# Kernel optimization log

Hardware: AMD Instinct MI355X
Metric: run time of the kernel (lower is better)

## Reference

```python
import jax, jax.numpy as jnp
import numpy as np

CH = 128
GROUPS = 8
HEADS = 8
HEAD_DIM = CH // HEADS  # 16
EPS = 1e-5


def setup_inputs() -> dict:
    key = jax.random.key(0)
    ks = jax.random.split(key, 5)
    x = jax.random.normal(ks[0], (8, CH, 128, 128), dtype=jnp.float32)
    gn_w = jnp.ones((CH,), dtype=jnp.float32)
    gn_b = jnp.zeros((CH,), dtype=jnp.float32)
    w_in = jax.random.normal(ks[1], (CH, CH), dtype=jnp.float32) * (1.0 / np.sqrt(CH))
    b_in = jax.random.normal(ks[2], (CH,), dtype=jnp.float32) * 0.01
    w_out = jax.random.normal(ks[3], (CH, CH), dtype=jnp.float32) * (1.0 / np.sqrt(CH))
    b_out = jax.random.normal(ks[4], (CH,), dtype=jnp.float32) * 0.01
    return {"x": x, "gn_w": gn_w, "gn_b": gn_b, "w_in": w_in, "b_in": b_in,
            "w_out": w_out, "b_out": b_out}


def _group_norm(x, gamma, beta):
    b, c, H, W = x.shape
    xg = x.reshape(b, GROUPS, c // GROUPS, H, W)
    mean = xg.mean(axis=(2, 3, 4), keepdims=True)
    var = xg.var(axis=(2, 3, 4), keepdims=True)
    xg = (xg - mean) * jax.lax.rsqrt(var + EPS)
    x = xg.reshape(b, c, H, W)
    return x * gamma[None, :, None, None] + beta[None, :, None, None]


def _conv1x1(x, w, bias):
    # w: [out_c, in_c] (1x1 conv == pointwise matmul over channels)
    return jnp.einsum('oc,bchw->bohw', w, x) + bias[None, :, None, None]


def reference(x, gn_w, gn_b, w_in, b_in, w_out, b_out):
    b, c, H, W = x.shape
    h = _group_norm(x, gn_w, gn_b)
    h = _conv1x1(h, w_in, b_in)
    # reshape to [b, heads, head_dim, H*W]; attention over head_dim axis,
    # contracting the spatial axis (d = H*W) as in the original einsums
    hh = h.reshape(b, HEADS, HEAD_DIM, H * W)
    scale = HEAD_DIM ** (-0.5)
    scores = jnp.einsum('bhid,bhjd->bhij', hh, hh) * scale  # [b,heads,hd,hd]
    weights = jax.nn.softmax(scores, axis=-1)
    attn = jnp.einsum('bhij,bhjd->bhid', weights, hh)
    attn = attn.reshape(b, c, H, W)
    h = _conv1x1(attn, w_out, b_out)
    return x + h
```

## Files before the change

kernel.cpp:

```cpp
#include <hip/hip_runtime.h>


#define NPOS 16384

typedef short short8 __attribute__((ext_vector_type(8)));
typedef float f32x4 __attribute__((ext_vector_type(4)));

__device__ __forceinline__ unsigned short f2bf(float f) {
    union { float f; unsigned u; } v; v.f = f;
    unsigned r = (v.u + 0x7fffu + ((v.u >> 16) & 1u)) >> 16;
    return (unsigned short)r;
}
__device__ __forceinline__ float bf2f(unsigned short u) {
    union { unsigned u; float f; } v; v.u = ((unsigned)u) << 16;
    return v.f;
}

__global__ __launch_bounds__(256, 2) void k_gram(const float* __restrict__ x,
                                                 float* __restrict__ G,
                                                 float* __restrict__ mv) {
    __shared__ unsigned short Xs[128 * 256];

    const int t = threadIdx.x;
    const int lane = t & 63, wv = t >> 6;
    const int q = lane >> 4, i16 = lane & 15;
    const int b = blockIdx.x >> 6;
    const int d0 = (blockIdx.x & 63) << 8;

    const float* xb = x + (size_t)b * (128 * NPOS) + d0;
#pragma unroll
    for (int i = 0; i < 32; ++i) {
        int idx = t + i * 256;
        int c = idx >> 6, d4 = idx & 63;
        float4 v = *((const float4*)(xb + (size_t)c * NPOS) + d4);
        ushort4 o;
        o.x = f2bf(v.x); o.y = f2bf(v.y); o.z = f2bf(v.z); o.w = f2bf(v.w);
        int g = d4 >> 1;
        int sg = g ^ (c & 7);
        *(ushort4*)&Xs[c * 256 + (sg << 3) + ((d4 & 1) << 2)] = o;
    }
    __syncthreads();

    f32x4 acc[2][8];
    f32x4 macc[2];
#pragma unroll
    for (int a = 0; a < 2; ++a) {
        macc[a] = (f32x4){0.f, 0.f, 0.f, 0.f};
#pragma unroll
        for (int ct = 0; ct < 8; ++ct) acc[a][ct] = (f32x4){0.f, 0.f, 0.f, 0.f};
    }
    const short8 ones = {(short)0x3F80, (short)0x3F80, (short)0x3F80, (short)0x3F80,
                         (short)0x3F80, (short)0x3F80, (short)0x3F80, (short)0x3F80};
    const int r0 = wv * 32 + i16, r1 = r0 + 16;
#pragma unroll
    for (int ks = 0; ks < 8; ++ks) {
        int g = ks * 4 + q;
        short8 a0 = *(const short8*)&Xs[r0 * 256 + ((g ^ (r0 & 7)) << 3)];
        short8 a1 = *(const short8*)&Xs[r1 * 256 + ((g ^ (r1 & 7)) << 3)];
        macc[0] = __builtin_amdgcn_mfma_f32_16x16x32_bf16(a0, ones, macc[0], 0, 0, 0);
        macc[1] = __builtin_amdgcn_mfma_f32_16x16x32_bf16(a1, ones, macc[1], 0, 0, 0);
#pragma unroll
        for (int ct = 0; ct < 8; ++ct) {
            int rb = ct * 16 + i16;
            short8 bb = *(const short8*)&Xs[rb * 256 + ((g ^ (rb & 7)) << 3)];
            acc[0][ct] = __builtin_amdgcn_mfma_f32_16x16x32_bf16(a0, bb, acc[0][ct], 0, 0, 0);
            acc[1][ct] = __builtin_amdgcn_mfma_f32_16x16x32_bf16(a1, bb, acc[1][ct], 0, 0, 0);
        }
    }

    float* Gb = G + b * 16384;
#pragma unroll
    for (int a = 0; a < 2; ++a) {
        int rb = wv * 32 + a * 16 + q * 4;
#pragma unroll
        for (int ct = 0; ct < 8; ++ct)
#pragma unroll
            for (int r = 0; r < 4; ++r)
                atomicAdd(&Gb[(rb + r) * 128 + ct * 16 + i16], acc[a][ct][r]);
        if (i16 == 0) {
#pragma unroll
            for (int r = 0; r < 4; ++r)
                atomicAdd(&mv[b * 128 + rb + r], macc[a][r]);
        }
    }
}

__global__ __launch_bounds__(512, 1) void k_fold(
    const float* __restrict__ G, const float* __restrict__ mv,
    const float* __restrict__ gn_w, const float* __restrict__ gn_b,
    const float* __restrict__ w_in, const float* __restrict__ b_in,
    const float* __restrict__ w_out, const float* __restrict__ b_out,
    unsigned short* __restrict__ Mb, float* __restrict__ bias2) {
    __shared__ unsigned short As[128 * 136];
    __shared__ float T2f[128 * 132];
    __shared__ float sW[8 * 16 * 16];
    __shared__ float sm[128], ss[128], st[128], sv[128], su[128], t2v[128];
    __shared__ float red[8][128];

    unsigned short* Ts = (unsigned short*)T2f;

    const int t = threadIdx.x;
    const int lane = t & 63, wv = t >> 6;
    const int q = lane >> 4, i16 = lane & 15;
    const int b = blockIdx.x;
    const float* Gb = G + b * 16384;

    if (t < 128) sm[t] = mv[b * 128 + t];
    __syncthreads();
    if (t < 128) {
        int g = t >> 4;
        float s1 = 0.f, s2 = 0.f;
#pragma unroll
        for (int k = 0; k < 16; ++k) {
            int c = g * 16 + k;
            s1 += sm[c];
            s2 += Gb[c * 128 + c];
        }
        const float invN = 1.0f / 262144.0f;
        float mean = s1 * invN;
        float var = s2 * invN - mean * mean;
        float rstd = rsqrtf(var + 1e-5f);
        float s = gn_w[t] * rstd;
        ss[t] = s;
        st[t] = gn_b[t] - mean * s;
    }
    __syncthreads();

    {
        int c = t & 127, quarter = t >> 7;
        float v = 0.f, u = 0.f;
        const float* wr = w_in + c * 128 + quarter * 32;
        unsigned short* ar = &As[c * 136 + quarter * 32];
#pragma unroll
        for (int k = 0; k < 32; ++k) {
            int kg = quarter * 32 + k;
            float w = wr[k];
            float a = w * ss[kg];
            ar[k] = f2bf(a);
            v += w * st[kg];
            u += a * sm[kg];
        }
        red[quarter][c] = v;
        red[4 + quarter][c] = u;
    }
    for (int idx = t; idx < 16384; idx += 512)
        Ts[(idx >> 7) * 136 + (idx & 127)] = f2bf(Gb[idx]);
    __syncthreads();
    if (t < 128) {
        sv[t] = b_in[t] + red[0][t] + red[1][t] + red[2][t] + red[3][t];
        su[t] = red[4][t] + red[5][t] + red[6][t] + red[7][t];
    }
    __syncthreads();

    f32x4 tacc[8];
#pragma unroll
    for (int ct = 0; ct < 8; ++ct) tacc[ct] = (f32x4){0.f, 0.f, 0.f, 0.f};
    const int rA = wv * 16 + i16;
#pragma unroll
    for (int ks = 0; ks < 4; ++ks) {
        short8 af = *(const short8*)&As[rA * 136 + ks * 32 + q * 8];
#pragma unroll
        for (int ct = 0; ct < 8; ++ct) {
            short8 gb = *(const short8*)&Ts[(ct * 16 + i16) * 136 + ks * 32 + q * 8];
            tacc[ct] = __builtin_amdgcn_mfma_f32_16x16x32_bf16(af, gb, tacc[ct], 0, 0, 0);
        }
    }
    __syncthreads();
#pragma unroll
    for (int ct = 0; ct < 8; ++ct)
#pragma unroll
        for (int r = 0; r < 4; ++r)
            Ts[(wv * 16 + q * 4 + r) * 136 + ct * 16 + i16] = f2bf(tacc[ct][r]);
    __syncthreads();

    {
        f32x4 sacc = (f32x4){0.f, 0.f, 0.f, 0.f};
#pragma unroll
        for (int ks = 0; ks < 4; ++ks) {
            short8 tf = *(const short8*)&Ts[rA * 136 + ks * 32 + q * 8];
            short8 af = *(const short8*)&As[rA * 136 + ks * 32 + q * 8];
            sacc = __builtin_amdgcn_mfma_f32_16x16x32_bf16(tf, af, sacc, 0, 0, 0);
        }
        int J = wv * 16 + i16;
        float vJ = sv[J], uJ = su[J];
#pragma unroll
        for (int r = 0; r < 4; ++r) {
            int I = wv * 16 + q * 4 + r;
            float val = (sacc[r] + su[I] * vJ + sv[I] * uJ + 16384.f * sv[I] * vJ) * 0.25f;
            float mx = val;
#pragma unroll
            for (int msk = 1; msk < 16; msk <<= 1) mx = fmaxf(mx, __shfl_xor(mx, msk));
            float e = __expf(val - mx);
            float sum = e;
#pragma unroll
            for (int msk = 1; msk < 16; msk <<= 1) sum += __shfl_xor(sum, msk);
            sW[(wv * 16 + q * 4 + r) * 16 + i16] = e / sum;
        }
    }
    __syncthreads();

    {
        int o = t & 127, quarter = t >> 7;
        int h = o >> 4, ii = o & 15;
        float a32[32];
#pragma unroll
        for (int kk = 0; kk < 32; ++kk) a32[kk] = 0.f;
#pragma unroll
        for (int j = 0; j < 16; ++j) {
            float wj = sW[(h * 16 + ii) * 16 + j];
            const ushort4* ar4 = (const ushort4*)&As[(h * 16 + j) * 136 + quarter * 32];
#pragma unroll
            for (int k4 = 0; k4 < 8; ++k4) {
                ushort4 vv = ar4[k4];
                a32[k4 * 4 + 0] += wj * bf2f(vv.x);
                a32[k4 * 4 + 1] += wj * bf2f(vv.y);
                a32[k4 * 4 + 2] += wj * bf2f(vv.z);
                a32[k4 * 4 + 3] += wj * bf2f(vv.w);
            }
        }
#pragma unroll
        for (int kk = 0; kk < 32; ++kk) T2f[o * 132 + quarter * 32 + kk] = a32[kk];
        if (t < 128) {
            float a = 0.f;
#pragma unroll
            for (int j = 0; j < 16; ++j) a += sW[(h * 16 + ii) * 16 + j] * sv[h * 16 + j];
            t2v[t] = a;
        }
    }
    __syncthreads();

    {
        int c = t & 127, quarter = t >> 7;
        float accM[32];
#pragma unroll
        for (int kk = 0; kk < 32; ++kk) accM[kk] = 0.f;
        const float* wor = w_out + c * 128;
        for (int o = 0; o < 128; ++o) {
            float w = wor[o];
            const float4* t2r = (const float4*)&T2f[o * 132 + quarter * 32];
#pragma unroll
            for (int k4 = 0; k4 < 8; ++k4) {
                float4 vv = t2r[k4];
                accM[k4 * 4 + 0] += w * vv.x;
                accM[k4 * 4 + 1] += w * vv.y;
                accM[k4 * 4 + 2] += w * vv.z;
                accM[k4 * 4 + 3] += w * vv.w;
            }
        }
        unsigned short* mrow = Mb + (size_t)b * 16384 + c * 128 + quarter * 32;
#pragma unroll
        for (int kk = 0; kk < 32; ++kk) mrow[kk] = f2bf(accM[kk]);
        if (t < 128) {
            float a = b_out[t];
            const float* wr = w_out + t * 128;
#pragma unroll
            for (int o = 0; o < 128; ++o) a += wr[o] * t2v[o];
            bias2[b * 128 + t] = a;
        }
    }
}

__global__ __launch_bounds__(256, 4) void k_out(const float* __restrict__ x,
                                                const unsigned short* __restrict__ Mb,
                                                const float* __restrict__ bias2,
                                                float* __restrict__ out) {
    __shared__ unsigned short Xt[128 * 128];
    __shared__ float b2s[128];

    const int t = threadIdx.x;
    const int lane = t & 63, wv = t >> 6;
    const int q = lane >> 4, i16 = lane & 15;
    const int b = blockIdx.x >> 7;
    const int p0 = (blockIdx.x & 127) << 7;

    if (t < 128) b2s[t] = bias2[b * 128 + t];

    const float* xb = x + (size_t)b * (128 * NPOS) + p0;
#pragma unroll
    for (int i = 0; i < 16; ++i) {
        int p = ((i & 1) << 6) + lane;
        int kq = (wv << 3) + (i >> 1);
        const float* col = xb + (size_t)(kq * 4) * NPOS + p;
        float a0 = col[0];
        float a1 = col[NPOS];
        float a2 = col[2 * NPOS];
        float a3 = col[3 * NPOS];
        ushort4 o; o.x = f2bf(a0); o.y = f2bf(a1); o.z = f2bf(a2); o.w = f2bf(a3);
        int g = kq >> 1;
        int sg = g ^ (p & 7);
        *(ushort4*)&Xt[p * 128 + (sg << 3) + ((kq & 1) << 2)] = o;
    }
    __syncthreads();

    f32x4 acc[2][8];
#pragma unroll
    for (int a = 0; a < 2; ++a)
#pragma unroll
        for (int pt = 0; pt < 8; ++pt) acc[a][pt] = (f32x4){0.f, 0.f, 0.f, 0.f};

    const unsigned short* Mrow = Mb + (size_t)b * 16384;
#pragma unroll
    for (int ks = 0; ks < 4; ++ks) {
        short8 a0 = *(const short8*)&Mrow[(wv * 32 + i16) * 128 + ks * 32 + q * 8];
        short8 a1 = *(const short8*)&Mrow[(wv * 32 + 16 + i16) * 128 + ks * 32 + q * 8];
        int g = ks * 4 + q;
#pragma unroll
        for (int pt = 0; pt < 8; ++pt) {
            int pr = pt * 16 + i16;
            short8 bb = *(const short8*)&Xt[pr * 128 + ((g ^ (pr & 7)) << 3)];
            acc[0][pt] = __builtin_amdgcn_mfma_f32_16x16x32_bf16(a0, bb, acc[0][pt], 0, 0, 0);
            acc[1][pt] = __builtin_amdgcn_mfma_f32_16x16x32_bf16(a1, bb, acc[1][pt], 0, 0, 0);
        }
    }

    float* ob = out + (size_t)b * (128 * NPOS) + p0;
#pragma unroll
    for (int a = 0; a < 2; ++a) {
        int cb = wv * 32 + a * 16 + q * 4;
#pragma unroll
        for (int pt = 0; pt < 8; ++pt) {
            int p = pt * 16 + i16;
#pragma unroll
            for (int r = 0; r < 4; ++r) {
                int c = cb + r;
                ob[(size_t)c * NPOS + p] = acc[a][pt][r] + b2s[c] + xb[(size_t)c * NPOS + p];
            }
        }
    }
}

extern "C" void kernel_launch(void* const* d_in, const int* in_sizes, int n_in,
                              void* d_out, int out_size, void* d_ws, size_t ws_size,
                              hipStream_t stream) {
    const float* x    = (const float*)d_in[0];
    const float* gn_w = (const float*)d_in[1];
    const float* gn_b = (const float*)d_in[2];
    const float* w_in = (const float*)d_in[3];
    const float* b_in = (const float*)d_in[4];
    const float* w_out= (const float*)d_in[5];
    const float* b_out= (const float*)d_in[6];
    float* out = (float*)d_out;

    char* ws = (char*)d_ws;
    float* G              = (float*)(ws + 0);
    float* mv             = (float*)(ws + 524288);
    float* bias2          = (float*)(ws + 528384);
    unsigned short* Mb    = (unsigned short*)(ws + 532480);

    hipMemsetAsync(d_ws, 0, 528384, stream);
    k_gram<<<dim3(512), dim3(256), 0, stream>>>(x, G, mv);
    k_fold<<<dim3(8), dim3(512), 0, stream>>>(G, mv, gn_w, gn_b, w_in, b_in,
                                              w_out, b_out, Mb, bias2);
    k_out<<<dim3(1024), dim3(256), 0, stream>>>(x, Mb, bias2, out);
}
```

Measured before the change: 204.1 us.

## Fuse gram, fold and output stages into one cooperative kernel with grid syncs

Replaces the memset plus three separate launches with a single cooperative kernel of 256 blocks, one per 512-position slab per batch, separated by grid-wide syncs. The Gram reduction now writes per-block partials that are summed deterministically instead of using global atomics. The construction of the fused output matrix is spread across 64 blocks instead of 8. The output stage tiles 512 positions per block. This removes launch gaps and atomic contention, but it adds several grid barriers and a 16MB partial-sum workspace, and it runs about one large-LDS block per CU, so there is less latency hiding in the memory-bound phases.

```diff
diff --git a/kernel.cpp b/kernel.cpp
--- a/kernel.cpp
+++ b/kernel.cpp
@@ -1,4 +1,5 @@
 #include <hip/hip_runtime.h>
+#include <hip/hip_cooperative_groups.h>
 
 
 #define NPOS 16384
@@ -16,314 +17,330 @@
     return v.f;
 }
 
-__global__ __launch_bounds__(256, 2) void k_gram(const float* __restrict__ x,
-                                                 float* __restrict__ G,
-                                                 float* __restrict__ mv) {
-    __shared__ unsigned short Xs[128 * 256];
+__global__ __launch_bounds__(512, 2) void k_fused(
+    const float* __restrict__ x,
+    const float* __restrict__ gn_w, const float* __restrict__ gn_b,
+    const float* __restrict__ w_in, const float* __restrict__ b_in,
+    const float* __restrict__ w_out, const float* __restrict__ b_out,
+    float* __restrict__ out,
+    float* Gpart, float* mpart, float* G, float* mvG,
+    float* ssg, float* sWg, float* t2vg, float* bias2,
+    unsigned short* Mb) {
+
+    __shared__ __align__(16) unsigned char SH[131072];
+    __shared__ float b2s[128];
 
     const int t = threadIdx.x;
     const int lane = t & 63, wv = t >> 6;
     const int q = lane >> 4, i16 = lane & 15;
-    const int b = blockIdx.x >> 6;
-    const int d0 = (blockIdx.x & 63) << 8;
-
-    const float* xb = x + (size_t)b * (128 * NPOS) + d0;
-#pragma unroll
-    for (int i = 0; i < 32; ++i) {
-        int idx = t + i * 256;
-        int c = idx >> 6, d4 = idx & 63;
-        float4 v = *((const float4*)(xb + (size_t)c * NPOS) + d4);
-        ushort4 o;
-        o.x = f2bf(v.x); o.y = f2bf(v.y); o.z = f2bf(v.z); o.w = f2bf(v.w);
-        int g = d4 >> 1;
-        int sg = g ^ (c & 7);
-        *(ushort4*)&Xs[c * 256 + (sg << 3) + ((d4 & 1) << 2)] = o;
-    }
-    __syncthreads();
-
-    f32x4 acc[2][8];
-    f32x4 macc[2];
-#pragma unroll
-    for (int a = 0; a < 2; ++a) {
-        macc[a] = (f32x4){0.f, 0.f, 0.f, 0.f};
-#pragma unroll
-        for (int ct = 0; ct < 8; ++ct) acc[a][ct] = (f32x4){0.f, 0.f, 0.f, 0.f};
-    }
-    const short8 ones = {(short)0x3F80, (short)0x3F80, (short)0x3F80, (short)0x3F80,
-                         (short)0x3F80, (short)0x3F80, (short)0x3F80, (short)0x3F80};
-    const int r0 = wv * 32 + i16, r1 = r0 + 16;
-#pragma unroll
-    for (int ks = 0; ks < 8; ++ks) {
-        int g = ks * 4 + q;
-        short8 a0 = *(const short8*)&Xs[r0 * 256 + ((g ^ (r0 & 7)) << 3)];
-        short8 a1 = *(const short8*)&Xs[r1 * 256 + ((g ^ (r1 & 7)) << 3)];
-        macc[0] = __builtin_amdgcn_mfma_f32_16x16x32_bf16(a0, ones, macc[0], 0, 0, 0);
-        macc[1] = __builtin_amdgcn_mfma_f32_16x16x32_bf16(a1, ones, macc[1], 0, 0, 0);
-#pragma unroll
-        for (int ct = 0; ct < 8; ++ct) {
-            int rb = ct * 16 + i16;
-            short8 bb = *(const short8*)&Xs[rb * 256 + ((g ^ (rb & 7)) << 3)];
-            acc[0][ct] = __builtin_amdgcn_mfma_f32_16x16x32_bf16(a0, bb, acc[0][ct], 0, 0, 0);
-            acc[1][ct] = __builtin_amdgcn_mfma_f32_16x16x32_bf16(a1, bb, acc[1][ct], 0, 0, 0);
-        }
-    }
-
-    float* Gb = G + b * 16384;
-#pragma unroll
-    for (int a = 0; a < 2; ++a) {
-        int rb = wv * 32 + a * 16 + q * 4;
+    const int blk = blockIdx.x;
+    const int b = blk >> 5, slab = blk & 31;
+    const size_t d0 = (size_t)slab << 9;
+
+    cooperative_groups::grid_group grid = cooperative_groups::this_grid();
+
+    {
+        unsigned short* Xs = (unsigned short*)SH;
+        const float* xb = x + (size_t)b * (128 * NPOS) + d0;
+#pragma unroll
+        for (int i = 0; i < 32; ++i) {
+            int idx = t + i * 512;
+            int c = idx >> 7, d4 = idx & 127;
+            float4 v = *((const float4*)(xb + (size_t)c * NPOS) + d4);
+            ushort4 o;
+            o.x = f2bf(v.x); o.y = f2bf(v.y); o.z = f2bf(v.z); o.w = f2bf(v.w);
+            int g = d4 >> 1;
+            int sg = g ^ (c & 7);
+            *(ushort4*)&Xs[c * 512 + (sg << 3) + ((d4 & 1) << 2)] = o;
+        }
+        __syncthreads();
+
+        f32x4 acc[8];
+        f32x4 macc = (f32x4){0.f, 0.f, 0.f, 0.f};
+#pragma unroll
+        for (int ct = 0; ct < 8; ++ct) acc[ct] = (f32x4){0.f, 0.f, 0.f, 0.f};
+        const short8 ones = {(short)0x3F80, (short)0x3F80, (short)0x3F80, (short)0x3F80,
+                             (short)0x3F80, (short)0x3F80, (short)0x3F80, (short)0x3F80};
+        const int r0 = wv * 16 + i16;
+#pragma unroll
+        for (int ks = 0; ks < 16; ++ks) {
+            int gd = ks * 4 + q;
+            short8 af = *(const short8*)&Xs[r0 * 512 + ((gd ^ (r0 & 7)) << 3)];
+            macc = __builtin_amdgcn_mfma_f32_16x16x32_bf16(af, ones, macc, 0, 0, 0);
+#pragma unroll
+            for (int ct = 0; ct < 8; ++ct) {
+                int rb = ct * 16 + i16;
+                short8 bf = *(const short8*)&Xs[rb * 512 + ((gd ^ (rb & 7)) << 3)];
+                acc[ct] = __builtin_amdgcn_mfma_f32_16x16x32_bf16(af, bf, acc[ct], 0, 0, 0);
+            }
+        }
+        float* gp = Gpart + (size_t)blk * 16384;
 #pragma unroll
         for (int ct = 0; ct < 8; ++ct)
 #pragma unroll
             for (int r = 0; r < 4; ++r)
-                atomicAdd(&Gb[(rb + r) * 128 + ct * 16 + i16], acc[a][ct][r]);
+                gp[(wv * 16 + q * 4 + r) * 128 + ct * 16 + i16] = acc[ct][r];
         if (i16 == 0) {
 #pragma unroll
             for (int r = 0; r < 4; ++r)
-                atomicAdd(&mv[b * 128 + rb + r], macc[a][r]);
-        }
-    }
-}
-
-__global__ __launch_bounds__(512, 1) void k_fold(
-    const float* __restrict__ G, const float* __restrict__ mv,
-    const float* __restrict__ gn_w, const float* __restrict__ gn_b,
-    const float* __restrict__ w_in, const float* __restrict__ b_in,
-    const float* __restrict__ w_out, const float* __restrict__ b_out,
-    unsigned short* __restrict__ Mb, float* __restrict__ bias2) {
-    __shared__ unsigned short As[128 * 136];
-    __shared__ float T2f[128 * 132];
-    __shared__ float sW[8 * 16 * 16];
-    __shared__ float sm[128], ss[128], st[128], sv[128], su[128], t2v[128];
-    __shared__ float red[8][128];
-
-    unsigned short* Ts = (unsigned short*)T2f;
-
-    const int t = threadIdx.x;
-    const int lane = t & 63, wv = t >> 6;
-    const int q = lane >> 4, i16 = lane & 15;
-    const int b = blockIdx.x;
-    const float* Gb = G + b * 16384;
-
-    if (t < 128) sm[t] = mv[b * 128 + t];
-    __syncthreads();
-    if (t < 128) {
-        int g = t >> 4;
-        float s1 = 0.f, s2 = 0.f;
-#pragma unroll
-        for (int k = 0; k < 16; ++k) {
-            int c = g * 16 + k;
-            s1 += sm[c];
-            s2 += Gb[c * 128 + c];
-        }
-        const float invN = 1.0f / 262144.0f;
-        float mean = s1 * invN;
-        float var = s2 * invN - mean * mean;
-        float rstd = rsqrtf(var + 1e-5f);
-        float s = gn_w[t] * rstd;
-        ss[t] = s;
-        st[t] = gn_b[t] - mean * s;
-    }
-    __syncthreads();
+                mpart[blk * 128 + wv * 16 + q * 4 + r] = macc[r];
+        }
+    }
+    grid.sync();
 
     {
-        int c = t & 127, quarter = t >> 7;
-        float v = 0.f, u = 0.f;
-        const float* wr = w_in + c * 128 + quarter * 32;
-        unsigned short* ar = &As[c * 136 + quarter * 32];
-#pragma unroll
-        for (int k = 0; k < 32; ++k) {
-            int kg = quarter * 32 + k;
-            float w = wr[k];
-            float a = w * ss[kg];
-            ar[k] = f2bf(a);
-            v += w * st[kg];
-            u += a * sm[kg];
-        }
-        red[quarter][c] = v;
-        red[4 + quarter][c] = u;
-    }
-    for (int idx = t; idx < 16384; idx += 512)
-        Ts[(idx >> 7) * 136 + (idx & 127)] = f2bf(Gb[idx]);
-    __syncthreads();
-    if (t < 128) {
-        sv[t] = b_in[t] + red[0][t] + red[1][t] + red[2][t] + red[3][t];
-        su[t] = red[4][t] + red[5][t] + red[6][t] + red[7][t];
-    }
-    __syncthreads();
-
-    f32x4 tacc[8];
-#pragma unroll
-    for (int ct = 0; ct < 8; ++ct) tacc[ct] = (f32x4){0.f, 0.f, 0.f, 0.f};
-    const int rA = wv * 16 + i16;
-#pragma unroll
-    for (int ks = 0; ks < 4; ++ks) {
-        short8 af = *(const short8*)&As[rA * 136 + ks * 32 + q * 8];
-#pragma unroll
-        for (int ct = 0; ct < 8; ++ct) {
-            short8 gb = *(const short8*)&Ts[(ct * 16 + i16) * 136 + ks * 32 + q * 8];
-            tacc[ct] = __builtin_amdgcn_mfma_f32_16x16x32_bf16(af, gb, tacc[ct], 0, 0, 0);
-        }
-    }
-    __syncthreads();
-#pragma unroll
-    for (int ct = 0; ct < 8; ++ct)
-#pragma unroll
-        for (int r = 0; r < 4; ++r)
-            Ts[(wv * 16 + q * 4 + r) * 136 + ct * 16 + i16] = f2bf(tacc[ct][r]);
-    __syncthreads();
-
-    {
-        f32x4 sacc = (f32x4){0.f, 0.f, 0.f, 0.f};
+        float sum = 0.f;
+        size_t base = (size_t)(b * 32) * 16384 + slab * 512 + t;
+#pragma unroll 4
+        for (int s = 0; s < 32; ++s) sum += Gpart[base + (size_t)s * 16384];
+        G[b * 16384 + slab * 512 + t] = sum;
+        if (slab == 0 && t < 128) {
+            float ms = 0.f;
+#pragma unroll 4
+            for (int s = 0; s < 32; ++s) ms += mpart[(b * 32 + s) * 128 + t];
+            mvG[b * 128 + t] = ms;
+        }
+    }
+    grid.sync();
+
+    if (slab == 0) {
+        unsigned short* As = (unsigned short*)SH;
+        unsigned short* Ts = (unsigned short*)(SH + 34816);
+        float* sW  = (float*)(SH + 69632);
+        float* sm  = (float*)(SH + 77824);
+        float* ss  = (float*)(SH + 78336);
+        float* st  = (float*)(SH + 78848);
+        float* sv  = (float*)(SH + 79360);
+        float* su  = (float*)(SH + 79872);
+        float* red = (float*)(SH + 80384);
+        const float* Gb = G + b * 16384;
+
+        if (t < 128) sm[t] = mvG[b * 128 + t];
+        __syncthreads();
+        if (t < 128) {
+            int g = t >> 4;
+            float s1 = 0.f, s2 = 0.f;
+#pragma unroll
+            for (int k = 0; k < 16; ++k) {
+                int c = g * 16 + k;
+                s1 += sm[c];
+                s2 += Gb[c * 128 + c];
+            }
+            const float invN = 1.0f / 262144.0f;
+            float mean = s1 * invN;
+            float var = s2 * invN - mean * mean;
+            float rstd = rsqrtf(var + 1e-5f);
+            float s = gn_w[t] * rstd;
+            ss[t] = s;
+            st[t] = gn_b[t] - mean * s;
+            ssg[b * 128 + t] = s;
+        }
+        __syncthreads();
+
+        {
+            int c = t & 127, quarter = t >> 7;
+            float v = 0.f, u = 0.f;
+            const float* wr = w_in + c * 128 + quarter * 32;
+            unsigned short* ar = &As[c * 136 + quarter * 32];
+#pragma unroll
+            for (int k = 0; k < 32; ++k) {
+                int kg = quarter * 32 + k;
+                float w = wr[k];
+                float a = w * ss[kg];
+                ar[k] = f2bf(a);
+                v += w * st[kg];
+                u += a * sm[kg];
+            }
+            red[quarter * 128 + c] = v;
+            red[(4 + quarter) * 128 + c] = u;
+        }
+        for (int idx = t; idx < 16384; idx += 512)
+            Ts[(idx >> 7) * 136 + (idx & 127)] = f2bf(Gb[idx]);
+        __syncthreads();
+        if (t < 128) {
+            sv[t] = b_in[t] + red[t] + red[128 + t] + red[256 + t] + red[384 + t];
+            su[t] = red[512 + t] + red[640 + t] + red[768 + t] + red[896 + t];
+        }
+        __syncthreads();
+
+        f32x4 tacc[8];
+#pragma unroll
+        for (int ct = 0; ct < 8; ++ct) tacc[ct] = (f32x4){0.f, 0.f, 0.f, 0.f};
+        const int rA = wv * 16 + i16;
 #pragma unroll
         for (int ks = 0; ks < 4; ++ks) {
-            short8 tf = *(const short8*)&Ts[rA * 136 + ks * 32 + q * 8];
             short8 af = *(const short8*)&As[rA * 136 + ks * 32 + q * 8];
-            sacc = __builtin_amdgcn_mfma_f32_16x16x32_bf16(tf, af, sacc, 0, 0, 0);
-        }
-        int J = wv * 16 + i16;
-        float vJ = sv[J], uJ = su[J];
-#pragma unroll
-        for (int r = 0; r < 4; ++r) {
-            int I = wv * 16 + q * 4 + r;
-            float val = (sacc[r] + su[I] * vJ + sv[I] * uJ + 16384.f * sv[I] * vJ) * 0.25f;
-            float mx = val;
-#pragma unroll
-            for (int msk = 1; msk < 16; msk <<= 1) mx = fmaxf(mx, __shfl_xor(mx, msk));
-            float e = __expf(val - mx);
-            float sum = e;
-#pragma unroll
-            for (int msk = 1; msk < 16; msk <<= 1) sum += __shfl_xor(sum, msk);
-            sW[(wv * 16 + q * 4 + r) * 16 + i16] = e / sum;
-        }
-    }
-    __syncthreads();
-
-    {
-        int o = t & 127, quarter = t >> 7;
-        int h = o >> 4, ii = o & 15;
-        float a32[32];
-#pragma unroll
-        for (int kk = 0; kk < 32; ++kk) a32[kk] = 0.f;
-#pragma unroll
-        for (int j = 0; j < 16; ++j) {
-            float wj = sW[(h * 16 + ii) * 16 + j];
-            const ushort4* ar4 = (const ushort4*)&As[(h * 16 + j) * 136 + quarter * 32];
-#pragma unroll
-            for (int k4 = 0; k4 < 8; ++k4) {
-                ushort4 vv = ar4[k4];
-                a32[k4 * 4 + 0] += wj * bf2f(vv.x);
-                a32[k4 * 4 + 1] += wj * bf2f(vv.y);
-                a32[k4 * 4 + 2] += wj * bf2f(vv.z);
-                a32[k4 * 4 + 3] += wj * bf2f(vv.w);
-            }
-        }
-#pragma unroll
-        for (int kk = 0; kk < 32; ++kk) T2f[o * 132 + quarter * 32 + kk] = a32[kk];
+#pragma unroll
+            for (int ct = 0; ct < 8; ++ct) {
+                short8 gbf = *(const short8*)&Ts[(ct * 16 + i16) * 136 + ks * 32 + q * 8];
+                tacc[ct] = __builtin_amdgcn_mfma_f32_16x16x32_bf16(af, gbf, tacc[ct], 0, 0, 0);
+            }
+        }
+        __syncthreads();
+#pragma unroll
+        for (int ct = 0; ct < 8; ++ct)
+#pragma unroll
+            for (int r = 0; r < 4; ++r)
+                Ts[(wv * 16 + q * 4 + r) * 136 + ct * 16 + i16] = f2bf(tacc[ct][r]);
+        __syncthreads();
+
+        {
+            f32x4 sacc = (f32x4){0.f, 0.f, 0.f, 0.f};
+#pragma unroll
+            for (int ks = 0; ks < 4; ++ks) {
+                short8 tf = *(const short8*)&Ts[rA * 136 + ks * 32 + q * 8];
+                short8 af = *(const short8*)&As[rA * 136 + ks * 32 + q * 8];
+                sacc = __builtin_amdgcn_mfma_f32_16x16x32_bf16(tf, af, sacc, 0, 0, 0);
+            }
+            int J = wv * 16 + i16;
+            float vJ = sv[J], uJ = su[J];
+#pragma unroll
+            for (int r = 0; r < 4; ++r) {
+                int I = wv * 16 + q * 4 + r;
+                float val = (sacc[r] + su[I] * vJ + sv[I] * uJ + 16384.f * sv[I] * vJ) * 0.25f;
+                float mx = val;
+#pragma unroll
+                for (int msk = 1; msk < 16; msk <<= 1) mx = fmaxf(mx, __shfl_xor(mx, msk));
+                float e = __expf(val - mx);
+                float sum = e;
+#pragma unroll
+                for (int msk = 1; msk < 16; msk <<= 1) sum += __shfl_xor(sum, msk);
+                float wgt = e / sum;
+                sW[I * 16 + i16] = wgt;
+                sWg[b * 2048 + I * 16 + i16] = wgt;
+            }
+        }
+        __syncthreads();
         if (t < 128) {
+            int h = t >> 4;
             float a = 0.f;
 #pragma unroll
-            for (int j = 0; j < 16; ++j) a += sW[(h * 16 + ii) * 16 + j] * sv[h * 16 + j];
-            t2v[t] = a;
-        }
-    }
-    __syncthreads();
-
-    {
-        int c = t & 127, quarter = t >> 7;
-        float accM[32];
-#pragma unroll
-        for (int kk = 0; kk < 32; ++kk) accM[kk] = 0.f;
-        const float* wor = w_out + c * 128;
-        for (int o = 0; o < 128; ++o) {
-            float w = wor[o];
-            const float4* t2r = (const float4*)&T2f[o * 132 + quarter * 32];
-#pragma unroll
-            for (int k4 = 0; k4 < 8; ++k4) {
-                float4 vv = t2r[k4];
-                accM[k4 * 4 + 0] += w * vv.x;
-                accM[k4 * 4 + 1] += w * vv.y;
-                accM[k4 * 4 + 2] += w * vv.z;
-                accM[k4 * 4 + 3] += w * vv.w;
-            }
-        }
-        unsigned short* mrow = Mb + (size_t)b * 16384 + c * 128 + quarter * 32;
-#pragma unroll
-        for (int kk = 0; kk < 32; ++kk) mrow[kk] = f2bf(accM[kk]);
-        if (t < 128) {
+            for (int j = 0; j < 16; ++j) a += sW[t * 16 + j] * sv[h * 16 + j];
+            t2vg[b * 128 + t] = a;
+        }
+    }
+    grid.sync();
+
+    if ((blk & 3) == 0) {
+        int blkC = blk >> 2, bC = blkC >> 3, part = blkC & 7;
+        unsigned short* As = (unsigned short*)SH;
+        float* T2f = (float*)(SH + 34816);
+        float* sW  = (float*)(SH + 102400);
+        float* ssl = (float*)(SH + 110592);
+
+        for (int idx = t; idx < 2048; idx += 512) sW[idx] = sWg[bC * 2048 + idx];
+        if (t < 128) ssl[t] = ssg[bC * 128 + t];
+        __syncthreads();
+        {
+            int c = t & 127, quarter = t >> 7;
+            const float* wr = w_in + c * 128 + quarter * 32;
+            unsigned short* ar = &As[c * 136 + quarter * 32];
+#pragma unroll
+            for (int k = 0; k < 32; ++k) ar[k] = f2bf(wr[k] * ssl[quarter * 32 + k]);
+        }
+        __syncthreads();
+        {
+            int o = t & 127, quarter = t >> 7;
+            int h = o >> 4;
+            float a32[32];
+#pragma unroll
+            for (int kk = 0; kk < 32; ++kk) a32[kk] = 0.f;
+#pragma unroll
+            for (int j = 0; j < 16; ++j) {
+                float wj = sW[o * 16 + j];
+                const ushort4* ar4 = (const ushort4*)&As[(h * 16 + j) * 136 + quarter * 32];
+#pragma unroll
+                for (int k4 = 0; k4 < 8; ++k4) {
+                    ushort4 vv = ar4[k4];
+                    a32[k4 * 4 + 0] += wj * bf2f(vv.x);
+                    a32[k4 * 4 + 1] += wj * bf2f(vv.y);
+                    a32[k4 * 4 + 2] += wj * bf2f(vv.z);
+                    a32[k4 * 4 + 3] += wj * bf2f(vv.w);
+                }
+            }
+#pragma unroll
+            for (int kk = 0; kk < 32; ++kk) T2f[o * 132 + quarter * 32 + kk] = a32[kk];
+        }
+        __syncthreads();
+        {
+            int m0 = t * 4;
+            int c = part * 16 + (m0 >> 7), k = m0 & 127;
+            const float* wor = w_out + c * 128;
+            float a0 = 0.f, a1 = 0.f, a2 = 0.f, a3 = 0.f;
+#pragma unroll 4
+            for (int o = 0; o < 128; ++o) {
+                float w = wor[o];
+                float4 vv = *(const float4*)&T2f[o * 132 + k];
+                a0 += w * vv.x; a1 += w * vv.y; a2 += w * vv.z; a3 += w * vv.w;
+            }
+            ushort4 o4;
+            o4.x = f2bf(a0); o4.y = f2bf(a1); o4.z = f2bf(a2); o4.w = f2bf(a3);
+            *(ushort4*)&Mb[bC * 16384 + c * 128 + k] = o4;
+        }
+        if (part == 0 && t < 128) {
             float a = b_out[t];
             const float* wr = w_out + t * 128;
-#pragma unroll
-            for (int o = 0; o < 128; ++o) a += wr[o] * t2v[o];
+#pragma unroll 4
+            for (int o = 0; o < 128; ++o) a += wr[o] * t2vg[bC * 128 + o];
             bias2[b * 128 + t] = a;
         }
     }
-}
-
-__global__ __launch_bounds__(256, 4) void k_out(const float* __restrict__ x,
-                                                const unsigned short* __restrict__ Mb,
-                                                const float* __restrict__ bias2,
-                                                float* __restrict__ out) {
-    __shared__ unsigned short Xt[128 * 128];
-    __shared__ float b2s[128];
-
-    const int t = threadIdx.x;
-    const int lane = t & 63, wv = t >> 6;
-    const int q = lane >> 4, i16 = lane & 15;
-    const int b = blockIdx.x >> 7;
-    const int p0 = (blockIdx.x & 127) << 7;
-
-    if (t < 128) b2s[t] = bias2[b * 128 + t];
-
-    const float* xb = x + (size_t)b * (128 * NPOS) + p0;
-#pragma unroll
-    for (int i = 0; i < 16; ++i) {
-        int p = ((i & 1) << 6) + lane;
-        int kq = (wv << 3) + (i >> 1);
-        const float* col = xb + (size_t)(kq * 4) * NPOS + p;
-        float a0 = col[0];
-        float a1 = col[NPOS];
-        float a2 = col[2 * NPOS];
-        float a3 = col[3 * NPOS];
-        ushort4 o; o.x = f2bf(a0); o.y = f2bf(a1); o.z = f2bf(a2); o.w = f2bf(a3);
-        int g = kq >> 1;
-        int sg = g ^ (p & 7);
-        *(ushort4*)&Xt[p * 128 + (sg << 3) + ((kq & 1) << 2)] = o;
-    }
-    __syncthreads();
-
-    f32x4 acc[2][8];
-#pragma unroll
-    for (int a = 0; a < 2; ++a)
-#pragma unroll
-        for (int pt = 0; pt < 8; ++pt) acc[a][pt] = (f32x4){0.f, 0.f, 0.f, 0.f};
-
-    const unsigned short* Mrow = Mb + (size_t)b * 16384;
-#pragma unroll
-    for (int ks = 0; ks < 4; ++ks) {
-        short8 a0 = *(const short8*)&Mrow[(wv * 32 + i16) * 128 + ks * 32 + q * 8];
-        short8 a1 = *(const short8*)&Mrow[(wv * 32 + 16 + i16) * 128 + ks * 32 + q * 8];
-        int g = ks * 4 + q;
-#pragma unroll
-        for (int pt = 0; pt < 8; ++pt) {
-            int pr = pt * 16 + i16;
-            short8 bb = *(const short8*)&Xt[pr * 128 + ((g ^ (pr & 7)) << 3)];
-            acc[0][pt] = __builtin_amdgcn_mfma_f32_16x16x32_bf16(a0, bb, acc[0][pt], 0, 0, 0);
-            acc[1][pt] = __builtin_amdgcn_mfma_f32_16x16x32_bf16(a1, bb, acc[1][pt], 0, 0, 0);
-        }
-    }
-
-    float* ob = out + (size_t)b * (128 * NPOS) + p0;
-#pragma unroll
-    for (int a = 0; a < 2; ++a) {
-        int cb = wv * 32 + a * 16 + q * 4;
-#pragma unroll
-        for (int pt = 0; pt < 8; ++pt) {
-            int p = pt * 16 + i16;
-#pragma unroll
-            for (int r = 0; r < 4; ++r) {
-                int c = cb + r;
-                ob[(size_t)c * NPOS + p] = acc[a][pt][r] + b2s[c] + xb[(size_t)c * NPOS + p];
+    grid.sync();
+
+    {
+        unsigned short* Xt = (unsigned short*)SH;
+        if (t < 128) b2s[t] = bias2[b * 128 + t];
+        const float* xb = x + (size_t)b * (128 * NPOS) + d0;
+#pragma unroll
+        for (int i = 0; i < 32; ++i) {
+            int pch = i & 7, kq = (wv << 2) + (i >> 3);
+            int p = (pch << 6) + lane;
+            const float* col = xb + (size_t)(kq * 4) * NPOS + p;
+            float a0 = col[0];
+            float a1 = col[NPOS];
+            float a2 = col[2 * NPOS];
+            float a3 = col[3 * NPOS];
+            ushort4 o; o.x = f2bf(a0); o.y = f2bf(a1); o.z = f2bf(a2); o.w = f2bf(a3);
+            int g = kq >> 1;
+            int sg = g ^ (p & 7);
+            *(ushort4*)&Xt[p * 128 + (sg << 3) + ((kq & 1) << 2)] = o;
+        }
+        __syncthreads();
+
+        const int cband = wv & 3, ph = wv >> 2;
+        f32x4 acc[2][16];
+#pragma unroll
+        for (int a = 0; a < 2; ++a)
+#pragma unroll
+            for (int pt = 0; pt < 16; ++pt) acc[a][pt] = (f32x4){0.f, 0.f, 0.f, 0.f};
+
+        const unsigned short* Mrow = Mb + (size_t)b * 16384;
+#pragma unroll
+        for (int ks = 0; ks < 4; ++ks) {
+            short8 a0 = *(const short8*)&Mrow[(cband * 32 + i16) * 128 + ks * 32 + q * 8];
+            short8 a1 = *(const short8*)&Mrow[(cband * 32 + 16 + i16) * 128 + ks * 32 + q * 8];
+            int g = ks * 4 + q;
+#pragma unroll
+            for (int pt = 0; pt < 16; ++pt) {
+                int pr = ph * 256 + pt * 16 + i16;
+                short8 bb = *(const short8*)&Xt[pr * 128 + ((g ^ (pr & 7)) << 3)];
+                acc[0][pt] = __builtin_amdgcn_mfma_f32_16x16x32_bf16(a0, bb, acc[0][pt], 0, 0, 0);
+                acc[1][pt] = __builtin_amdgcn_mfma_f32_16x16x32_bf16(a1, bb, acc[1][pt], 0, 0, 0);
+            }
+        }
+
+        float* ob = out + (size_t)b * (128 * NPOS) + d0;
+#pragma unroll
+        for (int a = 0; a < 2; ++a) {
+            int cb = cband * 32 + a * 16 + q * 4;
+#pragma unroll
+            for (int pt = 0; pt < 16; ++pt) {
+                int p = ph * 256 + pt * 16 + i16;
+#pragma unroll
+                for (int r = 0; r < 4; ++r) {
+                    int c = cb + r;
+                    ob[(size_t)c * NPOS + p] = acc[a][pt][r] + b2s[c] + xb[(size_t)c * NPOS + p];
+                }
             }
         }
     }
@@ -342,14 +359,21 @@
     float* out = (float*)d_out;
 
     char* ws = (char*)d_ws;
-    float* G              = (float*)(ws + 0);
-    float* mv             = (float*)(ws + 524288);
-    float* bias2          = (float*)(ws + 528384);
-    unsigned short* Mb    = (unsigned short*)(ws + 532480);
-
-    hipMemsetAsync(d_ws, 0, 528384, stream);
-    k_gram<<<dim3(512), dim3(256), 0, stream>>>(x, G, mv);
-    k_fold<<<dim3(8), dim3(512), 0, stream>>>(G, mv, gn_w, gn_b, w_in, b_in,
-                                              w_out, b_out, Mb, bias2);
-    k_out<<<dim3(1024), dim3(256), 0, stream>>>(x, Mb, bias2, out);
+    float* Gpart          = (float*)(ws + 0);
+    float* mpart          = (float*)(ws + 16777216);
+    float* G              = (float*)(ws + 16908288);
+    float* mvG            = (float*)(ws + 17432576);
+    float* ssg            = (float*)(ws + 17436672);
+    float* sWg            = (float*)(ws + 17440768);
+    float* t2vg           = (float*)(ws + 17506304);
+    float* bias2          = (float*)(ws + 17510400);
+    unsigned short* Mb    = (unsigned short*)(ws + 17514496);
+
+    void* args[] = {(void*)&x, (void*)&gn_w, (void*)&gn_b, (void*)&w_in,
+                    (void*)&b_in, (void*)&w_out, (void*)&b_out, (void*)&out,
+                    (void*)&Gpart, (void*)&mpart, (void*)&G, (void*)&mvG,
+                    (void*)&ssg, (void*)&sWg, (void*)&t2vg, (void*)&bias2,
+                    (void*)&Mb};
+    hipLaunchCooperativeKernel((const void*)k_fused, dim3(256), dim3(512),
+                               args, 0, stream);
 }
```

Result: slower. 304.5 us (+49.2%).

## Replace Gram atomics with partial buffers plus reduce kernel; refold attention-output matrix via MFMA

Applied to the files above, without the earlier changes.

k_gram now stages each 256-column slab in two 128-column halves, which halves its LDS footprint. Each block writes its full 128x128 partial Gram and mean partials to a workspace buffer instead of doing global atomicAdds. A new k_reduce kernel sums the 64 partials per batch, and the memset is removed. In k_fold the composite matrix is reassociated: w_out is first multiplied by the softmax weights per head, then by the scaled w_in using MFMA, replacing two scalar FP32 loops. The cost is an extra 32MB of partial writes and reads plus one more kernel launch.

```diff
diff --git a/kernel.cpp b/kernel.cpp
--- a/kernel.cpp
+++ b/kernel.cpp
@@ -11,35 +11,18 @@
     unsigned r = (v.u + 0x7fffu + ((v.u >> 16) & 1u)) >> 16;
     return (unsigned short)r;
 }
-__device__ __forceinline__ float bf2f(unsigned short u) {
-    union { unsigned u; float f; } v; v.u = ((unsigned)u) << 16;
-    return v.f;
-}
 
 __global__ __launch_bounds__(256, 2) void k_gram(const float* __restrict__ x,
-                                                 float* __restrict__ G,
-                                                 float* __restrict__ mv) {
-    __shared__ unsigned short Xs[128 * 256];
+                                                 float* __restrict__ Gpart,
+                                                 float* __restrict__ mpart) {
+    __shared__ __align__(16) unsigned char SH[67584];
 
     const int t = threadIdx.x;
     const int lane = t & 63, wv = t >> 6;
     const int q = lane >> 4, i16 = lane & 15;
-    const int b = blockIdx.x >> 6;
-    const int d0 = (blockIdx.x & 63) << 8;
-
-    const float* xb = x + (size_t)b * (128 * NPOS) + d0;
-#pragma unroll
-    for (int i = 0; i < 32; ++i) {
-        int idx = t + i * 256;
-        int c = idx >> 6, d4 = idx & 63;
-        float4 v = *((const float4*)(xb + (size_t)c * NPOS) + d4);
-        ushort4 o;
-        o.x = f2bf(v.x); o.y = f2bf(v.y); o.z = f2bf(v.z); o.w = f2bf(v.w);
-        int g = d4 >> 1;
-        int sg = g ^ (c & 7);
-        *(ushort4*)&Xs[c * 256 + (sg << 3) + ((d4 & 1) << 2)] = o;
-    }
-    __syncthreads();
+    const int blk = blockIdx.x;
+    const int b = blk >> 6, slab = blk & 63;
+    const size_t d0 = (size_t)slab << 8;
 
     f32x4 acc[2][8];
     f32x4 macc[2];
@@ -51,53 +34,102 @@
     }
     const short8 ones = {(short)0x3F80, (short)0x3F80, (short)0x3F80, (short)0x3F80,
                          (short)0x3F80, (short)0x3F80, (short)0x3F80, (short)0x3F80};
+    const float* xb = x + (size_t)b * (128 * NPOS) + d0;
+    unsigned short* Xs = (unsigned short*)SH;
     const int r0 = wv * 32 + i16, r1 = r0 + 16;
-#pragma unroll
-    for (int ks = 0; ks < 8; ++ks) {
-        int g = ks * 4 + q;
-        short8 a0 = *(const short8*)&Xs[r0 * 256 + ((g ^ (r0 & 7)) << 3)];
-        short8 a1 = *(const short8*)&Xs[r1 * 256 + ((g ^ (r1 & 7)) << 3)];
-        macc[0] = __builtin_amdgcn_mfma_f32_16x16x32_bf16(a0, ones, macc[0], 0, 0, 0);
-        macc[1] = __builtin_amdgcn_mfma_f32_16x16x32_bf16(a1, ones, macc[1], 0, 0, 0);
-#pragma unroll
-        for (int ct = 0; ct < 8; ++ct) {
-            int rb = ct * 16 + i16;
-            short8 bb = *(const short8*)&Xs[rb * 256 + ((g ^ (rb & 7)) << 3)];
-            acc[0][ct] = __builtin_amdgcn_mfma_f32_16x16x32_bf16(a0, bb, acc[0][ct], 0, 0, 0);
-            acc[1][ct] = __builtin_amdgcn_mfma_f32_16x16x32_bf16(a1, bb, acc[1][ct], 0, 0, 0);
-        }
-    }
-
-    float* Gb = G + b * 16384;
-#pragma unroll
-    for (int a = 0; a < 2; ++a) {
-        int rb = wv * 32 + a * 16 + q * 4;
+
+    for (int cc = 0; cc < 2; ++cc) {
+        if (cc) __syncthreads();
+#pragma unroll
+        for (int i = 0; i < 16; ++i) {
+            int idx = t + i * 256;
+            int c = idx >> 5, d4 = idx & 31;
+            float4 v = *((const float4*)(xb + (size_t)c * NPOS + cc * 128) + d4);
+            ushort4 o;
+            o.x = f2bf(v.x); o.y = f2bf(v.y); o.z = f2bf(v.z); o.w = f2bf(v.w);
+            int g = d4 >> 1;
+            int sg = g ^ (c & 7);
+            *(ushort4*)&Xs[c * 128 + (sg << 3) + ((d4 & 1) << 2)] = o;
+        }
+        __syncthreads();
+#pragma unroll
+        for (int ks = 0; ks < 4; ++ks) {
+            int gd = ks * 4 + q;
+            short8 a0 = *(const short8*)&Xs[r0 * 128 + ((gd ^ (r0 & 7)) << 3)];
+            short8 a1 = *(const short8*)&Xs[r1 * 128 + ((gd ^ (r1 & 7)) << 3)];
+            macc[0] = __builtin_amdgcn_mfma_f32_16x16x32_bf16(a0, ones, macc[0], 0, 0, 0);
+            macc[1] = __builtin_amdgcn_mfma_f32_16x16x32_bf16(a1, ones, macc[1], 0, 0, 0);
+#pragma unroll
+            for (int ct = 0; ct < 8; ++ct) {
+                int rb = ct * 16 + i16;
+                short8 bb = *(const short8*)&Xs[rb * 128 + ((gd ^ (rb & 7)) << 3)];
+                acc[0][ct] = __builtin_amdgcn_mfma_f32_16x16x32_bf16(a0, bb, acc[0][ct], 0, 0, 0);
+                acc[1][ct] = __builtin_amdgcn_mfma_f32_16x16x32_bf16(a1, bb, acc[1][ct], 0, 0, 0);
+            }
+        }
+    }
+    if (i16 == 0) {
+#pragma unroll
+        for (int a = 0; a < 2; ++a)
+#pragma unroll
+            for (int r = 0; r < 4; ++r)
+                mpart[blk * 128 + wv * 32 + a * 16 + q * 4 + r] = macc[a][r];
+    }
+    __syncthreads();
+
+    float* Tf = (float*)SH;
+#pragma unroll
+    for (int a = 0; a < 2; ++a)
 #pragma unroll
         for (int ct = 0; ct < 8; ++ct)
 #pragma unroll
             for (int r = 0; r < 4; ++r)
-                atomicAdd(&Gb[(rb + r) * 128 + ct * 16 + i16], acc[a][ct][r]);
-        if (i16 == 0) {
-#pragma unroll
-            for (int r = 0; r < 4; ++r)
-                atomicAdd(&mv[b * 128 + rb + r], macc[a][r]);
-        }
+                Tf[(wv * 32 + a * 16 + q * 4 + r) * 132 + ct * 16 + i16] = acc[a][ct][r];
+    __syncthreads();
+    float4* gp = (float4*)(Gpart + (size_t)blk * 16384);
+#pragma unroll
+    for (int i = 0; i < 16; ++i) {
+        int fi = t + i * 256;
+        int row = fi >> 5, c4 = fi & 31;
+        gp[row * 32 + c4] = *(float4*)&Tf[row * 132 + c4 * 4];
+    }
+}
+
+__global__ __launch_bounds__(256) void k_reduce(const float* __restrict__ Gpart,
+                                                const float* __restrict__ mpart,
+                                                float* __restrict__ G,
+                                                float* __restrict__ mv) {
+    int t = threadIdx.x;
+    int fi = blockIdx.x * 256 + t;
+    int b = fi >> 12, off4 = fi & 4095;
+    const float4* Gp4 = (const float4*)Gpart;
+    float4 s = (float4){0.f, 0.f, 0.f, 0.f};
+#pragma unroll 8
+    for (int sl = 0; sl < 64; ++sl) {
+        float4 v = Gp4[(size_t)(b * 64 + sl) * 4096 + off4];
+        s.x += v.x; s.y += v.y; s.z += v.z; s.w += v.w;
+    }
+    ((float4*)G)[fi] = s;
+    if (blockIdx.x < 8 && t < 128) {
+        float ms = 0.f;
+#pragma unroll 8
+        for (int sl = 0; sl < 64; ++sl) ms += mpart[(blockIdx.x * 64 + sl) * 128 + t];
+        mv[blockIdx.x * 128 + t] = ms;
     }
 }
 
 __global__ __launch_bounds__(512, 1) void k_fold(
-    const float* __restrict__ G, const float* __restrict__ mv,
+    const float* __restrict__ G, const float* __restrict__ mvG,
     const float* __restrict__ gn_w, const float* __restrict__ gn_b,
     const float* __restrict__ w_in, const float* __restrict__ b_in,
     const float* __restrict__ w_out, const float* __restrict__ b_out,
     unsigned short* __restrict__ Mb, float* __restrict__ bias2) {
     __shared__ unsigned short As[128 * 136];
-    __shared__ float T2f[128 * 132];
-    __shared__ float sW[8 * 16 * 16];
-    __shared__ float sm[128], ss[128], st[128], sv[128], su[128], t2v[128];
+    __shared__ unsigned short At[128 * 136];
+    __shared__ unsigned short Ts[128 * 136];
+    __shared__ float sW[2048];
+    __shared__ float sm[128], ss[128], st[128], sv[128], su[128];
     __shared__ float red[8][128];
-
-    unsigned short* Ts = (unsigned short*)T2f;
 
     const int t = threadIdx.x;
     const int lane = t & 63, wv = t >> 6;
@@ -105,7 +137,7 @@
     const int b = blockIdx.x;
     const float* Gb = G + b * 16384;
 
-    if (t < 128) sm[t] = mv[b * 128 + t];
+    if (t < 128) sm[t] = mvG[b * 128 + t];
     __syncthreads();
     if (t < 128) {
         int g = t >> 4;
@@ -136,7 +168,9 @@
             int kg = quarter * 32 + k;
             float w = wr[k];
             float a = w * ss[kg];
-            ar[k] = f2bf(a);
+            unsigned short ab = f2bf(a);
+            ar[k] = ab;
+            At[kg * 136 + c] = ab;
             v += w * st[kg];
             u += a * sm[kg];
         }
@@ -161,8 +195,8 @@
         short8 af = *(const short8*)&As[rA * 136 + ks * 32 + q * 8];
 #pragma unroll
         for (int ct = 0; ct < 8; ++ct) {
-            short8 gb = *(const short8*)&Ts[(ct * 16 + i16) * 136 + ks * 32 + q * 8];
-            tacc[ct] = __builtin_amdgcn_mfma_f32_16x16x32_bf16(af, gb, tacc[ct], 0, 0, 0);
+            short8 gbf = *(const short8*)&Ts[(ct * 16 + i16) * 136 + ks * 32 + q * 8];
+            tacc[ct] = __builtin_amdgcn_mfma_f32_16x16x32_bf16(af, gbf, tacc[ct], 0, 0, 0);
         }
     }
     __syncthreads();
@@ -194,69 +228,55 @@
             float sum = e;
 #pragma unroll
             for (int msk = 1; msk < 16; msk <<= 1) sum += __shfl_xor(sum, msk);
-            sW[(wv * 16 + q * 4 + r) * 16 + i16] = e / sum;
+            sW[I * 16 + i16] = e / sum;
         }
     }
     __syncthreads();
 
     {
-        int o = t & 127, quarter = t >> 7;
-        int h = o >> 4, ii = o & 15;
-        float a32[32];
-#pragma unroll
-        for (int kk = 0; kk < 32; ++kk) a32[kk] = 0.f;
-#pragma unroll
-        for (int j = 0; j < 16; ++j) {
-            float wj = sW[(h * 16 + ii) * 16 + j];
-            const ushort4* ar4 = (const ushort4*)&As[(h * 16 + j) * 136 + quarter * 32];
-#pragma unroll
-            for (int k4 = 0; k4 < 8; ++k4) {
-                ushort4 vv = ar4[k4];
-                a32[k4 * 4 + 0] += wj * bf2f(vv.x);
-                a32[k4 * 4 + 1] += wj * bf2f(vv.y);
-                a32[k4 * 4 + 2] += wj * bf2f(vv.z);
-                a32[k4 * 4 + 3] += wj * bf2f(vv.w);
+        int c = t & 127, grp = t >> 7;
+        unsigned short* Ps = Ts;
+        float pb = 0.f;
+#pragma unroll
+        for (int hh = 0; hh < 2; ++hh) {
+            int h = grp * 2 + hh;
+            float wrow[16];
+#pragma unroll
+            for (int i = 0; i < 16; ++i) wrow[i] = w_out[c * 128 + h * 16 + i];
+#pragma unroll
+            for (int j = 0; j < 16; ++j) {
+                float val = 0.f;
+#pragma unroll
+                for (int i = 0; i < 16; ++i) val += wrow[i] * sW[(h * 16 + i) * 16 + j];
+                Ps[c * 136 + h * 16 + j] = f2bf(val);
+                pb += val * sv[h * 16 + j];
             }
         }
-#pragma unroll
-        for (int kk = 0; kk < 32; ++kk) T2f[o * 132 + quarter * 32 + kk] = a32[kk];
-        if (t < 128) {
-            float a = 0.f;
-#pragma unroll
-            for (int j = 0; j < 16; ++j) a += sW[(h * 16 + ii) * 16 + j] * sv[h * 16 + j];
-            t2v[t] = a;
-        }
-    }
-    __syncthreads();
+        red[grp][c] = pb;
+    }
+    __syncthreads();
+    if (t < 128)
+        bias2[b * 128 + t] = b_out[t] + red[0][t] + red[1][t] + red[2][t] + red[3][t];
 
     {
-        int c = t & 127, quarter = t >> 7;
-        float accM[32];
-#pragma unroll
-        for (int kk = 0; kk < 32; ++kk) accM[kk] = 0.f;
-        const float* wor = w_out + c * 128;
-        for (int o = 0; o < 128; ++o) {
-            float w = wor[o];
-            const float4* t2r = (const float4*)&T2f[o * 132 + quarter * 32];
-#pragma unroll
-            for (int k4 = 0; k4 < 8; ++k4) {
-                float4 vv = t2r[k4];
-                accM[k4 * 4 + 0] += w * vv.x;
-                accM[k4 * 4 + 1] += w * vv.y;
-                accM[k4 * 4 + 2] += w * vv.z;
-                accM[k4 * 4 + 3] += w * vv.w;
+        f32x4 macc[8];
+#pragma unroll
+        for (int ct = 0; ct < 8; ++ct) macc[ct] = (f32x4){0.f, 0.f, 0.f, 0.f};
+#pragma unroll
+        for (int ks = 0; ks < 4; ++ks) {
+            short8 pf = *(const short8*)&Ts[rA * 136 + ks * 32 + q * 8];
+#pragma unroll
+            for (int ct = 0; ct < 8; ++ct) {
+                short8 atf = *(const short8*)&At[(ct * 16 + i16) * 136 + ks * 32 + q * 8];
+                macc[ct] = __builtin_amdgcn_mfma_f32_16x16x32_bf16(pf, atf, macc[ct], 0, 0, 0);
             }
         }
-        unsigned short* mrow = Mb + (size_t)b * 16384 + c * 128 + quarter * 32;
-#pragma unroll
-        for (int kk = 0; kk < 32; ++kk) mrow[kk] = f2bf(accM[kk]);
-        if (t < 128) {
-            float a = b_out[t];
-            const float* wr = w_out + t * 128;
-#pragma unroll
-            for (int o = 0; o < 128; ++o) a += wr[o] * t2v[o];
-            bias2[b * 128 + t] = a;
-        }
+        unsigned short* mb = Mb + (size_t)b * 16384;
+#pragma unroll
+        for (int ct = 0; ct < 8; ++ct)
+#pragma unroll
+            for (int r = 0; r < 4; ++r)
+                mb[(wv * 16 + q * 4 + r) * 128 + ct * 16 + i16] = f2bf(macc[ct][r]);
     }
 }
 
@@ -342,14 +362,16 @@
     float* out = (float*)d_out;
 
     char* ws = (char*)d_ws;
-    float* G              = (float*)(ws + 0);
-    float* mv             = (float*)(ws + 524288);
-    float* bias2          = (float*)(ws + 528384);
-    unsigned short* Mb    = (unsigned short*)(ws + 532480);
-
-    hipMemsetAsync(d_ws, 0, 528384, stream);
-    k_gram<<<dim3(512), dim3(256), 0, stream>>>(x, G, mv);
-    k_fold<<<dim3(8), dim3(512), 0, stream>>>(G, mv, gn_w, gn_b, w_in, b_in,
+    float* Gpart          = (float*)(ws + 0);
+    float* mpart          = (float*)(ws + 33554432);
+    float* G              = (float*)(ws + 33816576);
+    float* mvG            = (float*)(ws + 34340864);
+    float* bias2          = (float*)(ws + 34344960);
+    unsigned short* Mb    = (unsigned short*)(ws + 34349056);
+
+    k_gram<<<dim3(512), dim3(256), 0, stream>>>(x, Gpart, mpart);
+    k_reduce<<<dim3(128), dim3(256), 0, stream>>>(Gpart, mpart, G, mvG);
+    k_fold<<<dim3(8), dim3(512), 0, stream>>>(G, mvG, gn_w, gn_b, w_in, b_in,
                                               w_out, b_out, Mb, bias2);
     k_out<<<dim3(1024), dim3(256), 0, stream>>>(x, Mb, bias2, out);
 }
```

Result: faster. 171.9 us (-15.8%).
